# Kernel optimization log

Hardware: AMD Instinct MI355X
Metric: run time of the kernel (lower is better)

## Reference

```python
import jax, jax.numpy as jnp
import numpy as np

EPS = 1e-12  # torch F.normalize eps


def _l2norm(v, axis):
    n = jnp.sqrt(jnp.sum(v * v, axis=axis, keepdims=True))
    return v / jnp.maximum(n, EPS)


def setup_inputs() -> dict:
    key = jax.random.key(0)
    k1, k2, k3 = jax.random.split(key, 3)
    N, D, H, W, K = 64, 256, 64, 64, 64
    x = jax.random.normal(k1, (N, D, H, W), dtype=jnp.float32)
    conv_weight = jax.random.normal(k2, (K, D), dtype=jnp.float32)
    centroids = jax.random.uniform(k3, (K, D), dtype=jnp.float32)
    return {"x": x, "conv_weight": conv_weight, "centroids": centroids}


def reference(x, conv_weight, centroids):
    # x: [N, D, H, W]; conv_weight: [K, D] (1x1 conv); centroids: [K, D]
    N, D, H, W = x.shape
    K = centroids.shape[0]
    x = _l2norm(x, axis=1)                       # descriptor-wise L2 norm over D
    xf = x.reshape(N, D, H * W)                  # [N, D, L]
    # 1x1 conv == matmul over channel dim: [N, K, L]
    logits = jnp.einsum('kd,ndl->nkl', conv_weight, xf)
    a = jax.nn.softmax(logits, axis=1)           # softmax over clusters
    # vlad[n,k,d] = sum_l a[n,k,l] * (x[n,d,l] - c[k,d])
    #            = (a @ x^T)[n,k,d] - (sum_l a[n,k,l]) * c[k,d]
    vlad = jnp.einsum('nkl,ndl->nkd', a, xf) - a.sum(axis=2)[:, :, None] * centroids[None]
    vlad = _l2norm(vlad, axis=2)                 # intra-normalization
    vlad = vlad.reshape(N, K * D)
    vlad = _l2norm(vlad, axis=1)                 # global L2 norm
    return vlad
```

## Files before the change

### kernel.cpp

```cpp
#include <hip/hip_runtime.h>

typedef unsigned short u16;
typedef short bf16x8 __attribute__((ext_vector_type(8)));
typedef float f32x4  __attribute__((ext_vector_type(4)));

#define NN 64
#define DD 256
#define LL 4096
#define KK 64
#define CHUNK 512
#define SUB 16
#define NSTEP 32
#define NCH 8
#define SSZ (KK*DD)
#define XDL_S 40
#define XLD_S 264
#define AKL_S 40

__device__ __forceinline__ u16 f2bf(float f) {
  union { float f; unsigned int i; } v; v.f = f;
  return (u16)((v.i + 0x8000u) >> 16);
}

__device__ __forceinline__ void load_lds16(const float* g, float* l) {
  auto gp = reinterpret_cast<const __attribute__((address_space(1))) unsigned int*>(
      reinterpret_cast<unsigned long long>(g));
  auto lp = reinterpret_cast<__attribute__((address_space(3))) unsigned int*>(
      reinterpret_cast<unsigned long long>(l));
  __builtin_amdgcn_global_load_lds(gp, lp, 16, 0, 0);
}

__global__ void zero_ws_kernel(float* __restrict__ p, int n4) {
  int i = blockIdx.x * 256 + threadIdx.x;
  if (i < n4) ((f32x4*)p)[i] = (f32x4){0.f, 0.f, 0.f, 0.f};
}

template <bool PARTIAL>
__global__ __launch_bounds__(256, 2) void netvlad_main(
    const float* __restrict__ xg, const float* __restrict__ wg,
    float* __restrict__ Sg, float* __restrict__ Ag) {
  __shared__ __align__(16) float raw[2][DD * SUB];
  __shared__ __align__(16) u16  x_ld[SUB * XLD_S];
  __shared__ __align__(16) u16  x_dl[DD * XDL_S];
  __shared__ __align__(16) u16  akl[KK * AKL_S];
  __shared__ float pnw[4][SUB];
  __shared__ float wsum[4][SUB];

  const int tid  = threadIdx.x;
  const int w    = tid >> 6;
  const int lane = tid & 63;
  const int quad = lane >> 4;
  const int l15  = lane & 15;
  const int dblk = tid >> 3;
  const int lp   = tid & 7;
  const int n    = blockIdx.x >> 3;
  const int ch   = blockIdx.x & 7;

  bf16x8 aw[8];
  {
    const float* wp = wg + (w * 16 + l15) * DD + quad * 8;
#pragma unroll
    for (int s = 0; s < 8; ++s) {
      f32x4 wa = *(const f32x4*)(wp + s * 32);
      f32x4 wb = *(const f32x4*)(wp + s * 32 + 4);
      bf16x8 t;
#pragma unroll
      for (int j = 0; j < 4; ++j) { t[j] = (short)f2bf(wa[j]); t[j + 4] = (short)f2bf(wb[j]); }
      aw[s] = t;
    }
  }

  f32x4 acc2[16];
#pragma unroll
  for (int i = 0; i < 16; ++i) acc2[i] = (f32x4){0.f, 0.f, 0.f, 0.f};
  float regAk[4] = {0.f, 0.f, 0.f, 0.f};

  const float* xcol = xg + (size_t)n * DD * LL + (size_t)ch * CHUNK;
  const size_t goff = (size_t)(lane >> 2) * LL + (lane & 3) * 4;

  {
    const float* gs = xcol + (size_t)(w * 64) * LL + goff;
    float* lb = &raw[0][(w * 64) * SUB];
#pragma unroll
    for (int j = 0; j < 4; ++j)
      load_lds16(gs + (size_t)(j * 16) * LL, lb + j * 16 * SUB);
  }
  __syncthreads();

  for (int s = 0; s < NSTEP; ++s) {
    const int buf = s & 1;
    if (s + 1 < NSTEP) {
      const float* gs = xcol + (s + 1) * SUB + (size_t)(w * 64) * LL + goff;
      float* lb = &raw[buf ^ 1][(w * 64) * SUB];
#pragma unroll
      for (int j = 0; j < 4; ++j)
        load_lds16(gs + (size_t)(j * 16) * LL, lb + j * 16 * SUB);
    }

    {
      const float* col = &raw[buf][(w * 64 + quad) * SUB + l15];
      float pj = 0.f;
#pragma unroll
      for (int i = 0; i < 16; ++i) { float v = col[i * 4 * SUB]; pj += v * v; }
      pj += __shfl_xor(pj, 16);
      pj += __shfl_xor(pj, 32);
      if (lane < 16) pnw[w][lane] = pj;
    }

    {
      const int labs = ((s & 1) << 4) + lp * 2;
      const float* rb = &raw[buf][0];
      bf16x8 c0, c1;
#pragma unroll
      for (int r = 0; r < 8; ++r) {
        int d = dblk * 8 + r;
        float2 v = *(const float2*)(rb + d * SUB + lp * 2);
        u16 a = f2bf(v.x), b = f2bf(v.y);
        c0[r] = (short)a; c1[r] = (short)b;
        *(unsigned int*)&x_dl[d * XDL_S + labs] = (unsigned int)a | ((unsigned int)b << 16);
      }
      *(bf16x8*)&x_ld[(lp * 2)     * XLD_S + dblk * 8] = c0;
      *(bf16x8*)&x_ld[(lp * 2 + 1) * XLD_S + dblk * 8] = c1;
    }
    __syncthreads();

    f32x4 acc1 = (f32x4){0.f, 0.f, 0.f, 0.f};
#pragma unroll
    for (int s8 = 0; s8 < 8; ++s8) {
      bf16x8 b = *(const bf16x8*)&x_ld[l15 * XLD_S + s8 * 32 + quad * 8];
      acc1 = __builtin_amdgcn_mfma_f32_16x16x32_bf16(aw[s8], b, acc1, 0, 0, 0);
    }
    float s4 = pnw[0][l15] + pnw[1][l15] + pnw[2][l15] + pnw[3][l15];
    float rno = rsqrtf(fmaxf(s4, 1e-24f));
    float e[4];
    float ps = 0.f;
#pragma unroll
    for (int r = 0; r < 4; ++r) { e[r] = __expf(acc1[r] * rno); ps += e[r]; }
    ps += __shfl_xor(ps, 16);
    ps += __shfl_xor(ps, 32);
    if (lane < 16) wsum[w][lane] = ps;
    __syncthreads();

    {
      float rs = 1.f / (wsum[0][l15] + wsum[1][l15] + wsum[2][l15] + wsum[3][l15]);
      float rr = rs * rno;
      int labs = ((s & 1) << 4) + l15;
#pragma unroll
      for (int r = 0; r < 4; ++r) {
        regAk[r] += e[r] * rs;
        akl[(w * 16 + quad * 4 + r) * AKL_S + labs] = f2bf(e[r] * rr);
      }
    }

    if (s & 1) {
      __syncthreads();
      const int kk = w * 16 + l15;
      bf16x8 aA = *(const bf16x8*)&akl[kk * AKL_S + quad * 8];
#pragma unroll
      for (int dt = 0; dt < 16; ++dt) {
        int d = dt * 16 + l15;
        bf16x8 bX = *(const bf16x8*)&x_dl[d * XDL_S + quad * 8];
        acc2[dt] = __builtin_amdgcn_mfma_f32_16x16x32_bf16(aA, bX, acc2[dt], 0, 0, 0);
      }
      __syncthreads();
    }
  }

  if (PARTIAL) {
    float* Sp = Sg + (size_t)blockIdx.x * SSZ;
#pragma unroll
    for (int dt = 0; dt < 16; ++dt)
#pragma unroll
      for (int r = 0; r < 4; ++r)
        Sp[(w * 16 + quad * 4 + r) * DD + dt * 16 + l15] = acc2[dt][r];
  } else {
    float* Sn = Sg + (size_t)n * SSZ;
#pragma unroll
    for (int dt = 0; dt < 16; ++dt)
#pragma unroll
      for (int r = 0; r < 4; ++r)
        atomicAdd(&Sn[(w * 16 + quad * 4 + r) * DD + dt * 16 + l15], acc2[dt][r]);
  }
#pragma unroll
  for (int o = 1; o <= 8; o <<= 1)
#pragma unroll
    for (int r = 0; r < 4; ++r) regAk[r] += __shfl_xor(regAk[r], o);
  if (l15 == 0) {
    if (PARTIAL) {
      float* Ap = Ag + (size_t)blockIdx.x * KK;
#pragma unroll
      for (int r = 0; r < 4; ++r) Ap[w * 16 + quad * 4 + r] = regAk[r];
    } else {
#pragma unroll
      for (int r = 0; r < 4; ++r) atomicAdd(&Ag[n * KK + w * 16 + quad * 4 + r], regAk[r]);
    }
  }
}

template <int NSL>
__global__ __launch_bounds__(256, 2) void netvlad_fin(
    const float* __restrict__ Sg, const float* __restrict__ Ag,
    const float* __restrict__ cg, float* __restrict__ outg) {
  __shared__ float wtot[4];
  const int n = blockIdx.x, tid = threadIdx.x;
  const int w = tid >> 6, lane = tid & 63;
  const float* Sb = Sg + (size_t)n * NSL * SSZ;
  const float* Ab = Ag + (size_t)n * NSL * KK;

  f32x4 v[16];
  float rk[16];
  float tot = 0.f;
#pragma unroll
  for (int i = 0; i < 16; ++i) {
    const int k = w * 16 + i;
    float Ak = 0.f;
#pragma unroll
    for (int sl = 0; sl < NSL; ++sl) Ak += Ab[sl * KK + k];
    f32x4 sacc = (f32x4){0.f, 0.f, 0.f, 0.f};
#pragma unroll
    for (int sl = 0; sl < NSL; ++sl)
      sacc += *(const f32x4*)&Sb[(size_t)sl * SSZ + k * DD + lane * 4];
    f32x4 c4 = *(const f32x4*)&cg[k * DD + lane * 4];
    f32x4 t = sacc - Ak * c4;
    v[i] = t;
    float q = t[0] * t[0] + t[1] * t[1] + t[2] * t[2] + t[3] * t[3];
#pragma unroll
    for (int o = 1; o <= 32; o <<= 1) q += __shfl_xor(q, o);
    float r = 1.f / fmaxf(sqrtf(q), 1e-12f);
    rk[i] = r;
    tot += q * r * r;
  }
  if (lane == 0) wtot[w] = tot;
  __syncthreads();
  const float g = wtot[0] + wtot[1] + wtot[2] + wtot[3];
  const float gs = 1.f / fmaxf(sqrtf(g), 1e-12f);
#pragma unroll
  for (int i = 0; i < 16; ++i) {
    const int k = w * 16 + i;
    const float sc = rk[i] * gs;
    f32x4 o = v[i];
    o[0] *= sc; o[1] *= sc; o[2] *= sc; o[3] *= sc;
    *(f32x4*)&outg[(size_t)n * SSZ + k * DD + lane * 4] = o;
  }
}

extern "C" void kernel_launch(void* const* d_in, const int* in_sizes, int n_in,
                              void* d_out, int out_size, void* d_ws, size_t ws_size,
                              hipStream_t stream) {
  const float* x   = (const float*)d_in[0];
  const float* wgt = (const float*)d_in[1];
  const float* cen = (const float*)d_in[2];
  float* out = (float*)d_out;

  const size_t nblk = (size_t)NN * NCH;
  const size_t need = nblk * SSZ * 4 + nblk * KK * 4;
  if (ws_size >= need) {
    float* Sp = (float*)d_ws;
    float* Ap = Sp + nblk * SSZ;
    hipLaunchKernelGGL((netvlad_main<true>), dim3(NN * NCH), dim3(256), 0, stream, x, wgt, Sp, Ap);
    hipLaunchKernelGGL((netvlad_fin<NCH>), dim3(NN), dim3(256), 0, stream, Sp, Ap, cen, out);
  } else {
    float* S = (float*)d_ws;
    float* A = S + (size_t)NN * SSZ;
    const int n4 = (NN * SSZ + NN * KK) / 4;
    hipLaunchKernelGGL(zero_ws_kernel, dim3((n4 + 255) / 256), dim3(256), 0, stream, S, n4);
    hipLaunchKernelGGL((netvlad_main<false>), dim3(NN * NCH), dim3(256), 0, stream, x, wgt, S, A);
    hipLaunchKernelGGL((netvlad_fin<1>), dim3(NN), dim3(256), 0, stream, S, A, cen, out);
  }
}
```

Baseline: 397.5 us.

## Prefetch x into registers and split second GEMM by D per wave

```diff
diff --git a/kernel.cpp b/kernel.cpp
--- a/kernel.cpp
+++ b/kernel.cpp
@@ -1,6 +1,7 @@
 #include <hip/hip_runtime.h>
 
 typedef unsigned short u16;
+typedef unsigned int u32;
 typedef short bf16x8 __attribute__((ext_vector_type(8)));
 typedef float f32x4  __attribute__((ext_vector_type(4)));
 
@@ -9,25 +10,21 @@
 #define LL 4096
 #define KK 64
 #define CHUNK 512
-#define SUB 16
-#define NSTEP 32
+#define SUB 32
+#define NSTEP 16
 #define NCH 8
 #define SSZ (KK*DD)
+#define XLD_S 264
 #define XDL_S 40
-#define XLD_S 264
 #define AKL_S 40
 
 __device__ __forceinline__ u16 f2bf(float f) {
-  union { float f; unsigned int i; } v; v.f = f;
+  union { float f; u32 i; } v; v.f = f;
   return (u16)((v.i + 0x8000u) >> 16);
 }
 
-__device__ __forceinline__ void load_lds16(const float* g, float* l) {
-  auto gp = reinterpret_cast<const __attribute__((address_space(1))) unsigned int*>(
-      reinterpret_cast<unsigned long long>(g));
-  auto lp = reinterpret_cast<__attribute__((address_space(3))) unsigned int*>(
-      reinterpret_cast<unsigned long long>(l));
-  __builtin_amdgcn_global_load_lds(gp, lp, 16, 0, 0);
+__device__ __forceinline__ void barrier_lds() {
+  asm volatile("s_waitcnt lgkmcnt(0)\n\ts_barrier" ::: "memory");
 }
 
 __global__ void zero_ws_kernel(float* __restrict__ p, int n4) {
@@ -39,10 +36,9 @@
 __global__ __launch_bounds__(256, 2) void netvlad_main(
     const float* __restrict__ xg, const float* __restrict__ wg,
     float* __restrict__ Sg, float* __restrict__ Ag) {
-  __shared__ __align__(16) float raw[2][DD * SUB];
-  __shared__ __align__(16) u16  x_ld[SUB * XLD_S];
-  __shared__ __align__(16) u16  x_dl[DD * XDL_S];
-  __shared__ __align__(16) u16  akl[KK * AKL_S];
+  __shared__ __align__(16) u16 x_ld[SUB * XLD_S];
+  __shared__ __align__(16) u16 x_dl[4][64 * XDL_S];
+  __shared__ __align__(16) u16 akl[KK * AKL_S];
   __shared__ float pnw[4][SUB];
   __shared__ float wsum[4][SUB];
 
@@ -51,8 +47,8 @@
   const int lane = tid & 63;
   const int quad = lane >> 4;
   const int l15  = lane & 15;
-  const int dblk = tid >> 3;
-  const int lp   = tid & 7;
+  const int g    = lane >> 3;
+  const int c    = lane & 7;
   const int n    = blockIdx.x >> 3;
   const int ch   = blockIdx.x & 7;
 
@@ -70,116 +66,136 @@
     }
   }
 
-  f32x4 acc2[16];
-#pragma unroll
-  for (int i = 0; i < 16; ++i) acc2[i] = (f32x4){0.f, 0.f, 0.f, 0.f};
+  f32x4 acc2[4][4];
+#pragma unroll
+  for (int a = 0; a < 4; ++a)
+#pragma unroll
+    for (int b = 0; b < 4; ++b) acc2[a][b] = (f32x4){0.f, 0.f, 0.f, 0.f};
   float regAk[4] = {0.f, 0.f, 0.f, 0.f};
 
-  const float* xcol = xg + (size_t)n * DD * LL + (size_t)ch * CHUNK;
-  const size_t goff = (size_t)(lane >> 2) * LL + (lane & 3) * 4;
-
-  {
-    const float* gs = xcol + (size_t)(w * 64) * LL + goff;
-    float* lb = &raw[0][(w * 64) * SUB];
-#pragma unroll
-    for (int j = 0; j < 4; ++j)
-      load_lds16(gs + (size_t)(j * 16) * LL, lb + j * 16 * SUB);
-  }
-  __syncthreads();
-
-  for (int s = 0; s < NSTEP; ++s) {
-    const int buf = s & 1;
+  const float* xw = xg + (size_t)n * DD * LL + (size_t)(w * 64 + g * 8) * LL
+                    + ch * CHUNK + c * 4;
+
+  f32x4 buf0[8], buf1[8];
+#pragma unroll
+  for (int i = 0; i < 8; ++i) buf0[i] = *(const f32x4*)(xw + (size_t)i * LL);
+
+  auto step = [&](f32x4 (&cur)[8], f32x4 (&nxt)[8], int s) {
     if (s + 1 < NSTEP) {
-      const float* gs = xcol + (s + 1) * SUB + (size_t)(w * 64) * LL + goff;
-      float* lb = &raw[buf ^ 1][(w * 64) * SUB];
-#pragma unroll
-      for (int j = 0; j < 4; ++j)
-        load_lds16(gs + (size_t)(j * 16) * LL, lb + j * 16 * SUB);
+      const float* q = xw + (s + 1) * SUB;
+#pragma unroll
+      for (int i = 0; i < 8; ++i) nxt[i] = *(const f32x4*)(q + (size_t)i * LL);
     }
 
     {
-      const float* col = &raw[buf][(w * 64 + quad) * SUB + l15];
-      float pj = 0.f;
-#pragma unroll
-      for (int i = 0; i < 16; ++i) { float v = col[i * 4 * SUB]; pj += v * v; }
-      pj += __shfl_xor(pj, 16);
-      pj += __shfl_xor(pj, 32);
-      if (lane < 16) pnw[w][lane] = pj;
-    }
-
-    {
-      const int labs = ((s & 1) << 4) + lp * 2;
-      const float* rb = &raw[buf][0];
-      bf16x8 c0, c1;
-#pragma unroll
-      for (int r = 0; r < 8; ++r) {
-        int d = dblk * 8 + r;
-        float2 v = *(const float2*)(rb + d * SUB + lp * 2);
-        u16 a = f2bf(v.x), b = f2bf(v.y);
-        c0[r] = (short)a; c1[r] = (short)b;
-        *(unsigned int*)&x_dl[d * XDL_S + labs] = (unsigned int)a | ((unsigned int)b << 16);
+      f32x4 pj = (f32x4){0.f, 0.f, 0.f, 0.f};
+#pragma unroll
+      for (int i = 0; i < 8; ++i) pj += cur[i] * cur[i];
+#pragma unroll
+      for (int o = 8; o <= 32; o <<= 1)
+#pragma unroll
+        for (int j = 0; j < 4; ++j) pj[j] += __shfl_xor(pj[j], o);
+      if (g == 0) *(f32x4*)&pnw[w][c * 4] = pj;
+    }
+
+    u16 xb[8][4];
+#pragma unroll
+    for (int i = 0; i < 8; ++i)
+#pragma unroll
+      for (int j = 0; j < 4; ++j) xb[i][j] = f2bf(cur[i][j]);
+#pragma unroll
+    for (int i = 0; i < 8; ++i) {
+      u32 lo = (u32)xb[i][0] | ((u32)xb[i][1] << 16);
+      u32 hi = (u32)xb[i][2] | ((u32)xb[i][3] << 16);
+      *(uint2*)&x_dl[w][(g * 8 + i) * XDL_S + c * 4] = make_uint2(lo, hi);
+    }
+#pragma unroll
+    for (int j = 0; j < 4; ++j) {
+      bf16x8 col;
+#pragma unroll
+      for (int i = 0; i < 8; ++i) col[i] = (short)xb[i][j];
+      *(bf16x8*)&x_ld[(c * 4 + j) * XLD_S + w * 64 + g * 8] = col;
+    }
+    barrier_lds();
+
+    f32x4 acc1[2];
+    acc1[0] = (f32x4){0.f, 0.f, 0.f, 0.f};
+    acc1[1] = (f32x4){0.f, 0.f, 0.f, 0.f};
+#pragma unroll
+    for (int s8 = 0; s8 < 8; ++s8)
+#pragma unroll
+      for (int lt = 0; lt < 2; ++lt) {
+        bf16x8 b = *(const bf16x8*)&x_ld[(lt * 16 + l15) * XLD_S + s8 * 32 + quad * 8];
+        acc1[lt] = __builtin_amdgcn_mfma_f32_16x16x32_bf16(aw[s8], b, acc1[lt], 0, 0, 0);
       }
-      *(bf16x8*)&x_ld[(lp * 2)     * XLD_S + dblk * 8] = c0;
-      *(bf16x8*)&x_ld[(lp * 2 + 1) * XLD_S + dblk * 8] = c1;
-    }
-    __syncthreads();
-
-    f32x4 acc1 = (f32x4){0.f, 0.f, 0.f, 0.f};
-#pragma unroll
-    for (int s8 = 0; s8 < 8; ++s8) {
-      bf16x8 b = *(const bf16x8*)&x_ld[l15 * XLD_S + s8 * 32 + quad * 8];
-      acc1 = __builtin_amdgcn_mfma_f32_16x16x32_bf16(aw[s8], b, acc1, 0, 0, 0);
-    }
-    float s4 = pnw[0][l15] + pnw[1][l15] + pnw[2][l15] + pnw[3][l15];
-    float rno = rsqrtf(fmaxf(s4, 1e-24f));
-    float e[4];
-    float ps = 0.f;
-#pragma unroll
-    for (int r = 0; r < 4; ++r) { e[r] = __expf(acc1[r] * rno); ps += e[r]; }
-    ps += __shfl_xor(ps, 16);
-    ps += __shfl_xor(ps, 32);
-    if (lane < 16) wsum[w][lane] = ps;
-    __syncthreads();
-
-    {
-      float rs = 1.f / (wsum[0][l15] + wsum[1][l15] + wsum[2][l15] + wsum[3][l15]);
-      float rr = rs * rno;
-      int labs = ((s & 1) << 4) + l15;
+    float rno[2], e[2][4], ps[2];
+#pragma unroll
+    for (int lt = 0; lt < 2; ++lt) {
+      int col = lt * 16 + l15;
+      float s4 = pnw[0][col] + pnw[1][col] + pnw[2][col] + pnw[3][col];
+      rno[lt] = rsqrtf(fmaxf(s4, 1e-24f));
+      float p = 0.f;
+#pragma unroll
+      for (int r = 0; r < 4; ++r) { e[lt][r] = __expf(acc1[lt][r] * rno[lt]); p += e[lt][r]; }
+      p += __shfl_xor(p, 16);
+      p += __shfl_xor(p, 32);
+      ps[lt] = p;
+    }
+    if (quad < 2) wsum[w][quad * 16 + l15] = (quad == 0) ? ps[0] : ps[1];
+    barrier_lds();
+
+#pragma unroll
+    for (int lt = 0; lt < 2; ++lt) {
+      int col = lt * 16 + l15;
+      float rs = 1.f / (wsum[0][col] + wsum[1][col] + wsum[2][col] + wsum[3][col]);
+      float rr = rs * rno[lt];
 #pragma unroll
       for (int r = 0; r < 4; ++r) {
-        regAk[r] += e[r] * rs;
-        akl[(w * 16 + quad * 4 + r) * AKL_S + labs] = f2bf(e[r] * rr);
+        regAk[r] += e[lt][r] * rs;
+        akl[(w * 16 + quad * 4 + r) * AKL_S + col] = f2bf(e[lt][r] * rr);
       }
     }
-
-    if (s & 1) {
-      __syncthreads();
-      const int kk = w * 16 + l15;
-      bf16x8 aA = *(const bf16x8*)&akl[kk * AKL_S + quad * 8];
-#pragma unroll
-      for (int dt = 0; dt < 16; ++dt) {
-        int d = dt * 16 + l15;
-        bf16x8 bX = *(const bf16x8*)&x_dl[d * XDL_S + quad * 8];
-        acc2[dt] = __builtin_amdgcn_mfma_f32_16x16x32_bf16(aA, bX, acc2[dt], 0, 0, 0);
-      }
-      __syncthreads();
-    }
+    barrier_lds();
+
+    bf16x8 bx[4];
+#pragma unroll
+    for (int dt = 0; dt < 4; ++dt)
+      bx[dt] = *(const bf16x8*)&x_dl[w][(dt * 16 + l15) * XDL_S + quad * 8];
+#pragma unroll
+    for (int kt = 0; kt < 4; ++kt) {
+      bf16x8 aA = *(const bf16x8*)&akl[(kt * 16 + l15) * AKL_S + quad * 8];
+#pragma unroll
+      for (int dt = 0; dt < 4; ++dt)
+        acc2[kt][dt] = __builtin_amdgcn_mfma_f32_16x16x32_bf16(aA, bx[dt], acc2[kt][dt], 0, 0, 0);
+    }
+    barrier_lds();
+  };
+
+#pragma unroll 1
+  for (int sp = 0; sp < NSTEP / 2; ++sp) {
+    step(buf0, buf1, 2 * sp);
+    step(buf1, buf0, 2 * sp + 1);
   }
 
   if (PARTIAL) {
     float* Sp = Sg + (size_t)blockIdx.x * SSZ;
 #pragma unroll
-    for (int dt = 0; dt < 16; ++dt)
-#pragma unroll
-      for (int r = 0; r < 4; ++r)
-        Sp[(w * 16 + quad * 4 + r) * DD + dt * 16 + l15] = acc2[dt][r];
+    for (int kt = 0; kt < 4; ++kt)
+#pragma unroll
+      for (int dt = 0; dt < 4; ++dt)
+#pragma unroll
+        for (int r = 0; r < 4; ++r)
+          Sp[(kt * 16 + quad * 4 + r) * DD + w * 64 + dt * 16 + l15] = acc2[kt][dt][r];
   } else {
     float* Sn = Sg + (size_t)n * SSZ;
 #pragma unroll
-    for (int dt = 0; dt < 16; ++dt)
-#pragma unroll
-      for (int r = 0; r < 4; ++r)
-        atomicAdd(&Sn[(w * 16 + quad * 4 + r) * DD + dt * 16 + l15], acc2[dt][r]);
+    for (int kt = 0; kt < 4; ++kt)
+#pragma unroll
+      for (int dt = 0; dt < 4; ++dt)
+#pragma unroll
+        for (int r = 0; r < 4; ++r)
+          atomicAdd(&Sn[(kt * 16 + quad * 4 + r) * DD + w * 64 + dt * 16 + l15],
+                    acc2[kt][dt][r]);
   }
 #pragma unroll
   for (int o = 1; o <= 8; o <<= 1)
@@ -232,8 +248,8 @@
   }
   if (lane == 0) wtot[w] = tot;
   __syncthreads();
-  const float g = wtot[0] + wtot[1] + wtot[2] + wtot[3];
-  const float gs = 1.f / fmaxf(sqrtf(g), 1e-12f);
+  const float gtot = wtot[0] + wtot[1] + wtot[2] + wtot[3];
+  const float gs = 1.f / fmaxf(sqrtf(gtot), 1e-12f);
 #pragma unroll
   for (int i = 0; i < 16; ++i) {
     const int k = w * 16 + i;
```

After: 394.1 us. About the same (-0.8%).
